# Optimization experiments

Measured on AMD Instinct MI355X. Metric: run time of the kernel, lower is better.

## Reference

```python
import jax, jax.numpy as jnp
import numpy as np

B, DIM_IN, DIM_OUT, K, SPK, T = 16, 256, 256, 5, 128, 8192
PAD = (K // 2, K // 2)  # odd kernel -> symmetric reflect pad


def setup_inputs() -> dict:
    key = jax.random.key(0)
    k1, k2, k3, k4 = jax.random.split(key, 4)
    x = jax.random.normal(k1, (B, DIM_IN, T), dtype=jnp.float32)
    c_trg = jax.random.normal(k2, (B, SPK), dtype=jnp.float32)
    # EqualLinear params (bias_init=1, lr_mul=1; forward uses raw weight, no scale)
    style_w = jax.random.normal(k3, (DIM_IN, SPK), dtype=jnp.float32)
    style_b = jnp.ones((DIM_IN,), dtype=jnp.float32)
    # base conv weight [1, dim_out, dim_in, k]
    weight = jax.random.normal(k4, (1, DIM_OUT, DIM_IN, K), dtype=jnp.float32)
    return {"x": x, "c_trg": c_trg, "style_w": style_w, "style_b": style_b, "weight": weight}


def _modulated_conv(x, c_trg, style_w, style_b, weight):
    # style: [B, dim_in]
    s = c_trg @ style_w.T + style_b
    # modulate: [B, dim_out, dim_in, K]
    w = weight * s[:, None, :, None]
    demod = jax.lax.rsqrt(jnp.sum(w * w, axis=(2, 3)) + 1e-8)  # [B, dim_out]
    w = w * demod[:, :, None, None]
    # reflect pad along time
    x_pad = jnp.pad(x, ((0, 0), (0, 0), PAD), mode="reflect")
    # per-sample conv1d (groups=batch in torch) via vmap
    def conv_one(xi, wi):
        # xi: [dim_in, T+K-1], wi: [dim_out, dim_in, K]
        out = jax.lax.conv_general_dilated(
            xi[None], wi, window_strides=(1,), padding="VALID",
            dimension_numbers=("NCH", "OIH", "NCH"))
        return out[0]  # [dim_out, T]
    out = jax.vmap(conv_one)(x_pad, w)
    return jax.nn.leaky_relu(out, negative_slope=0.2)


def reference(x, c_trg, style_w, style_b, weight):
    out = _modulated_conv(x, c_trg, style_w, style_b, weight)
    return (out, c_trg)
```

## Files before the change

kernel.cpp:

```cpp
#include <hip/hip_runtime.h>


#define B_    16
#define CIN   256
#define COUT  256
#define KW    5
#define SPK   128
#define TT    8192

#define OM    128
#define TN    256
#define BI    32
#define NCH   (CIN / BI)

#define XROWS 264
#define WSLAB (KW * OM * 32)
#define WBF_BYTES ((size_t)2 * NCH * WSLAB * 2)
#define S_OFF   WBF_BYTES
#define DM_OFF  (WBF_BYTES + (size_t)B_ * CIN * 4)
#define WS_NEED (WBF_BYTES + (size_t)B_ * CIN * 4 * 2)

typedef __attribute__((ext_vector_type(8))) short short8;
typedef __attribute__((ext_vector_type(4))) float f32x4;
typedef unsigned short ushort_t;
typedef unsigned int uint_t;

__device__ __forceinline__ ushort_t f2bf(float f) {
    uint_t u = __float_as_uint(f);
    u += 0x7FFF + ((u >> 16) & 1);
    return (ushort_t)(u >> 16);
}

__global__ __launch_bounds__(256) void prep2_kernel(
    const float* __restrict__ c_trg, const float* __restrict__ style_w,
    const float* __restrict__ style_b, const float* __restrict__ weight,
    ushort_t* __restrict__ wbf, float* __restrict__ s_glob,
    float* __restrict__ dm_glob)
{
    __shared__ float sm[8 * 1280];
    __shared__ float c_sh[SPK];
    __shared__ float s2_sh[CIN];

    const int tid = threadIdx.x;

    if (blockIdx.x < 32) {
        const int og = blockIdx.x;
        const float* wsrc = weight + (size_t)og * 8 * 1280;
        #pragma unroll
        for (int it = 0; it < 10; ++it)
            *(float4*)&sm[(it * 256 + tid) * 4] = *(const float4*)&wsrc[(it * 256 + tid) * 4];
        __syncthreads();

        for (int r = tid; r < 320; r += 256) {
            const int oi  = r / 40;
            const int rem = r - oi * 40;
            const int ch  = rem / 5;
            const int k   = rem - ch * 5;
            const int o   = og * 8 + oi;
            const int ot  = o >> 7;
            const int o_l = o & 127;
            const int swz = (o_l >> 1) & 3;
            ushort_t* dst = wbf + (((size_t)(ot * NCH + ch) * KW + k) * OM + o_l) * 32;
            #pragma unroll
            for (int g = 0; g < 4; ++g) {
                union { ushort_t us[8]; uint4 v; } pk;
                #pragma unroll
                for (int ii = 0; ii < 8; ++ii) {
                    int i_g = ch * 32 + g * 8 + ii;
                    pk.us[ii] = f2bf(sm[oi * 1280 + i_g * 5 + k]);
                }
                *(uint4*)&dst[(g ^ swz) * 8] = pk.v;
            }
        }
    } else {
        const int b = blockIdx.x - 32;
        if (tid < SPK) c_sh[tid] = c_trg[b * SPK + tid];
        __syncthreads();

        float acc = style_b[tid];
        const float* wr = style_w + (size_t)tid * SPK;
        #pragma unroll 4
        for (int j = 0; j < SPK; ++j) acc += c_sh[j] * wr[j];
        s_glob[b * CIN + tid] = acc;
        s2_sh[tid] = acc * acc;
        __syncthreads();

        const float* wo = weight + (size_t)tid * 1280;
        float a = 0.f;
        #pragma unroll 4
        for (int ig = 0; ig < 64; ++ig) {
            float q[20];
            #pragma unroll
            for (int f = 0; f < 5; ++f)
                *(float4*)&q[f * 4] = *(const float4*)&wo[ig * 20 + f * 4];
            #pragma unroll
            for (int c = 0; c < 4; ++c) {
                const float s2 = s2_sh[ig * 4 + c];
                #pragma unroll
                for (int k = 0; k < 5; ++k) {
                    const float v = q[c * 5 + k];
                    a += v * v * s2;
                }
            }
        }
        dm_glob[b * COUT + tid] = rsqrtf(a + 1e-8f);
    }
}

__global__ __launch_bounds__(512, 2) void conv_mfma_ws4_kernel(
    const float* __restrict__ x, const ushort_t* __restrict__ wbf,
    const float* __restrict__ s_glob, const float* __restrict__ dm_glob,
    float* __restrict__ out)
{
    __shared__ __align__(16) ushort_t w_sh[2][WSLAB];
    __shared__ __align__(16) ushort_t x_sh[XROWS * 32];
    __shared__ float s_lds[CIN];
    __shared__ float dm_lds[OM];

    const int b   = blockIdx.z;
    const int ot  = blockIdx.y;
    const int o0  = ot * OM;
    const int t0  = blockIdx.x * TN;
    const int tid = threadIdx.x;

    const int lane  = tid & 63;
    const int wv    = tid >> 6;
    const int wm    = wv >> 2;
    const int wn    = wv & 3;
    const int col16 = lane & 15;
    const int quad  = lane >> 4;

    const int rl = lane;
    const int i4 = wv;

    f32x4 acc[4][4];
    #pragma unroll
    for (int mt = 0; mt < 4; ++mt)
        #pragma unroll
        for (int nt = 0; nt < 4; ++nt)
            acc[mt][nt] = (f32x4){0.f, 0.f, 0.f, 0.f};

    const float* xb = x + (size_t)b * CIN * TT;
    const ushort_t* wslab = wbf + (size_t)ot * NCH * WSLAB;

    float xr0[20], xr1[20];

#define STAGE_W(CH, BUF) do {                                                  \
        const ushort_t* ws_ = wslab + (size_t)(CH) * WSLAB;                    \
        _Pragma("unroll")                                                      \
        for (int s_ = 0; s_ < 5; ++s_) {                                       \
            const int off_ = s_ * 4096 + wv * 512;           \
            __builtin_amdgcn_global_load_lds(                                  \
                (const __attribute__((address_space(1))) uint_t*)(ws_ + off_ + lane * 8), \
                (__attribute__((address_space(3))) uint_t*)(&w_sh[BUF][off_]), \
                16, 0, 0);                                                     \
        }                                                                      \
    } while (0)

#define LOAD_X(CH, XR) do {                                                    \
        const float* xp_ = xb + (size_t)((CH) * BI + i4 * 4) * TT;             \
        _Pragma("unroll")                                                      \
        for (int rd_ = 0; rd_ < 5; ++rd_) {                                    \
            int r_ = rd_ * 64 + rl;                                            \
            if (r_ < 260) {                                                    \
                int tg_ = t0 + r_ - 2;                                         \
                tg_ = (tg_ < 0) ? -tg_ : tg_;                                  \
                tg_ = (tg_ > TT - 1) ? (2 * (TT - 1) - tg_) : tg_;             \
                XR[rd_ * 4 + 0] = xp_[tg_];                                    \
                XR[rd_ * 4 + 1] = xp_[TT + tg_];                               \
                XR[rd_ * 4 + 2] = xp_[2 * TT + tg_];                           \
                XR[rd_ * 4 + 3] = xp_[3 * TT + tg_];                           \
            }                                                                  \
        }                                                                      \
    } while (0)

#define PUT_X(CH, XR) do {                                                     \
        const float s0_ = s_lds[(CH) * BI + i4 * 4 + 0];                       \
        const float s1_ = s_lds[(CH) * BI + i4 * 4 + 1];                       \
        const float s2_ = s_lds[(CH) * BI + i4 * 4 + 2];                       \
        const float s3_ = s_lds[(CH) * BI + i4 * 4 + 3];                       \
        _Pragma("unroll")                                                      \
        for (int rd_ = 0; rd_ < 5; ++rd_) {                                    \
            int r_ = rd_ * 64 + rl;                                            \
            if (r_ < 260) {                                                    \
                union { ushort_t us[4]; uint2 u2; } p_;                        \
                p_.us[0] = f2bf(XR[rd_ * 4 + 0] * s0_);                        \
                p_.us[1] = f2bf(XR[rd_ * 4 + 1] * s1_);                        \
                p_.us[2] = f2bf(XR[rd_ * 4 + 2] * s2_);                        \
                p_.us[3] = f2bf(XR[rd_ * 4 + 3] * s3_);                        \
                int grp_ = (i4 >> 1) ^ ((r_ ^ (r_ >> 2)) & 3);                 \
                *(uint2*)&x_sh[r_ * 32 + grp_ * 8 + (i4 & 1) * 4] = p_.u2;     \
            }                                                                  \
        }                                                                      \
    } while (0)

#define MFMA_CHUNK(BUF) do {                                                   \
        _Pragma("unroll")                                                      \
        for (int kt_ = 0; kt_ < KW; ++kt_) {                                   \
            short8 a_[4], bf_[4];                                              \
            _Pragma("unroll")                                                  \
            for (int mt_ = 0; mt_ < 4; ++mt_) {                                \
                const int row_  = kt_ * OM + wm * 64 + mt_ * 16 + col16;       \
                const int slot_ = quad ^ ((row_ >> 1) & 3);                    \
                a_[mt_] = *(const short8*)&w_sh[BUF][row_ * 32 + slot_ * 8];   \
            }                                                                  \
            _Pragma("unroll")                                                  \
            for (int nt_ = 0; nt_ < 4; ++nt_) {                                \
                const int r_   = wn * 64 + nt_ * 16 + col16 + kt_;             \
                const int grp_ = quad ^ ((r_ ^ (r_ >> 2)) & 3);                \
                bf_[nt_] = *(const short8*)&x_sh[r_ * 32 + grp_ * 8];          \
            }                                                                  \
            _Pragma("unroll")                                                  \
            for (int mt_ = 0; mt_ < 4; ++mt_)                                  \
                _Pragma("unroll")                                              \
                for (int nt_ = 0; nt_ < 4; ++nt_)                              \
                    acc[mt_][nt_] = __builtin_amdgcn_mfma_f32_16x16x32_bf16(   \
                        a_[mt_], bf_[nt_], acc[mt_][nt_], 0, 0, 0);            \
        }                                                                      \
    } while (0)

#define CHUNK_BODY(CH, CUR, NXT, XR_CUR, XR_NXT) do {                          \
        PUT_X(CH, XR_CUR);                                                     \
        __syncthreads();                                                       \
        if ((CH) < NCH - 1) {                                                  \
            STAGE_W((CH) + 1, NXT);                                            \
            LOAD_X((CH) + 1, XR_NXT);                                          \
        }                                                                      \
        __builtin_amdgcn_sched_barrier(0);                                     \
        MFMA_CHUNK(CUR);                                                       \
        if ((CH) < NCH - 1)                                                    \
            __syncthreads();                                                   \
    } while (0)

    if (tid < CIN) s_lds[tid] = s_glob[b * CIN + tid];
    if (tid < OM)  dm_lds[tid] = dm_glob[b * COUT + o0 + tid];
    STAGE_W(0, 0);
    LOAD_X(0, xr0);
    __syncthreads();

    CHUNK_BODY(0, 0, 1, xr0, xr1);
    CHUNK_BODY(1, 1, 0, xr1, xr0);
    CHUNK_BODY(2, 0, 1, xr0, xr1);
    CHUNK_BODY(3, 1, 0, xr1, xr0);
    CHUNK_BODY(4, 0, 1, xr0, xr1);
    CHUNK_BODY(5, 1, 0, xr1, xr0);
    CHUNK_BODY(6, 0, 1, xr0, xr1);
    CHUNK_BODY(7, 1, 0, xr1, xr0);

#undef STAGE_W
#undef LOAD_X
#undef PUT_X
#undef MFMA_CHUNK
#undef CHUNK_BODY

    #pragma unroll
    for (int mt = 0; mt < 4; ++mt) {
        #pragma unroll
        for (int nt = 0; nt < 4; ++nt) {
            const int t_o = t0 + wn * 64 + nt * 16 + col16;
            #pragma unroll
            for (int reg = 0; reg < 4; ++reg) {
                const int o_l = wm * 64 + mt * 16 + quad * 4 + reg;
                float v = acc[mt][nt][reg] * dm_lds[o_l];
                v = (v > 0.f) ? v : 0.2f * v;
                out[((size_t)(b * COUT + o0 + o_l)) * TT + t_o] = v;
            }
        }
    }
}

__global__ __launch_bounds__(256, 3) void conv_mfma_fb_kernel(
    const float* __restrict__ x, const float* __restrict__ c_trg,
    const float* __restrict__ style_w, const float* __restrict__ style_b,
    const float* __restrict__ weight, float* __restrict__ out)
{
    __shared__ ushort_t x_sh[136 * 32];
    __shared__ ushort_t w_sh[KW * 128 * 32];
    __shared__ float    c_sh[SPK];
    __shared__ float    s_sh[CIN];
    __shared__ float    dm_acc[128];
    __shared__ float    dmv[128];

    const int b   = blockIdx.z;
    const int o0  = blockIdx.y * 128;
    const int t0  = blockIdx.x * 128;
    const int tid = threadIdx.x;

    const int lane  = tid & 63;
    const int wvv   = tid >> 6;
    const int wm    = wvv >> 1;
    const int wn    = wvv & 1;
    const int col16 = lane & 15;
    const int quad  = lane >> 4;

    if (tid < SPK) c_sh[tid] = c_trg[b * SPK + tid];
    if (tid < 128) dm_acc[tid] = 0.f;
    __syncthreads();
    {
        float acc = style_b[tid];
        const float* wr = style_w + (size_t)tid * SPK;
        #pragma unroll 4
        for (int j = 0; j < SPK; ++j) acc += c_sh[j] * wr[j];
        s_sh[tid] = acc;
    }

    f32x4 acc[4][4];
    #pragma unroll
    for (int mt = 0; mt < 4; ++mt)
        #pragma unroll
        for (int nt = 0; nt < 4; ++nt)
            acc[mt][nt] = (f32x4){0.f, 0.f, 0.f, 0.f};

    const float* xb = x + (size_t)b * CIN * TT;

    for (int ch = 0; ch < NCH; ++ch) {
        const int i0 = ch * BI;
        __syncthreads();
        {
            const int i4s = tid >> 5;
            const int rls = tid & 31;
            const float* xp = xb + (size_t)(i0 + i4s * 4) * TT;
            #pragma unroll
            for (int rr = 0; rr < 136; rr += 32) {
                int r = rr + rls;
                if (r < 136) {
                    int tg = t0 + r - 2;
                    tg = (tg < 0) ? -tg : tg;
                    tg = (tg > TT - 1) ? (2 * (TT - 1) - tg) : tg;
                    float v0 = xp[tg];
                    float v1 = xp[TT + tg];
                    float v2 = xp[2 * TT + tg];
                    float v3 = xp[3 * TT + tg];
                    union { ushort_t us[4]; uint2 u2; } p;
                    p.us[0] = f2bf(v0); p.us[1] = f2bf(v1);
                    p.us[2] = f2bf(v2); p.us[3] = f2bf(v3);
                    int grp = (i4s >> 1) ^ (r & 3);
                    *(uint2*)&x_sh[r * 32 + grp * 8 + (i4s & 1) * 4] = p.u2;
                }
            }
        }
        {
            const int i4s = tid & 7;
            #pragma unroll
            for (int pass = 0; pass < 4; ++pass) {
                const int o_l = (tid >> 3) + pass * 32;
                const float* wp = weight + ((size_t)(o0 + o_l) * CIN + i0 + i4s * 4) * KW;
                float q[20];
                #pragma unroll
                for (int f = 0; f < 5; ++f)
                    *(float4*)&q[f * 4] = *(const float4*)(wp + f * 4);
                float sv0 = s_sh[i0 + i4s * 4 + 0];
                float sv1 = s_sh[i0 + i4s * 4 + 1];
                float sv2 = s_sh[i0 + i4s * 4 + 2];
                float sv3 = s_sh[i0 + i4s * 4 + 3];
                float m0[5], m1[5], m2[5], m3[5];
                float psum = 0.f;
                #pragma unroll
                for (int k = 0; k < 5; ++k) {
                    m0[k] = q[0 * 5 + k] * sv0;  psum += m0[k] * m0[k];
                    m1[k] = q[1 * 5 + k] * sv1;  psum += m1[k] * m1[k];
                    m2[k] = q[2 * 5 + k] * sv2;  psum += m2[k] * m2[k];
                    m3[k] = q[3 * 5 + k] * sv3;  psum += m3[k] * m3[k];
                }
                atomicAdd(&dm_acc[o_l], psum);
                #pragma unroll
                for (int k = 0; k < 5; ++k) {
                    union { ushort_t us[4]; uint2 u2; } p;
                    p.us[0] = f2bf(m0[k]); p.us[1] = f2bf(m1[k]);
                    p.us[2] = f2bf(m2[k]); p.us[3] = f2bf(m3[k]);
                    *(uint2*)&w_sh[(k * 128 + o_l) * 32 + i4s * 4] = p.u2;
                }
            }
        }
        __syncthreads();
        #pragma unroll
        for (int kt = 0; kt < KW; ++kt) {
            short8 a[4], bf[4];
            #pragma unroll
            for (int mt = 0; mt < 4; ++mt)
                a[mt] = *(const short8*)&w_sh[(kt * 128 + wm * 64 + mt * 16 + col16) * 32 + quad * 8];
            #pragma unroll
            for (int nt = 0; nt < 4; ++nt) {
                int r   = wn * 64 + nt * 16 + col16 + kt;
                int grp = quad ^ (r & 3);
                bf[nt] = *(const short8*)&x_sh[r * 32 + grp * 8];
            }
            #pragma unroll
            for (int mt = 0; mt < 4; ++mt)
                #pragma unroll
                for (int nt = 0; nt < 4; ++nt)
                    acc[mt][nt] = __builtin_amdgcn_mfma_f32_16x16x32_bf16(
                        a[mt], bf[nt], acc[mt][nt], 0, 0, 0);
        }
    }

    __syncthreads();
    if (tid < 128) dmv[tid] = rsqrtf(dm_acc[tid] + 1e-8f);
    __syncthreads();

    #pragma unroll
    for (int mt = 0; mt < 4; ++mt) {
        #pragma unroll
        for (int nt = 0; nt < 4; ++nt) {
            const int t_o = t0 + wn * 64 + nt * 16 + col16;
            #pragma unroll
            for (int reg = 0; reg < 4; ++reg) {
                const int o_l = wm * 64 + mt * 16 + quad * 4 + reg;
                float v = acc[mt][nt][reg] * dmv[o_l];
                v = (v > 0.f) ? v : 0.2f * v;
                out[((size_t)(b * COUT + o0 + o_l)) * TT + t_o] = v;
            }
        }
    }
}

extern "C" void kernel_launch(void* const* d_in, const int* in_sizes, int n_in,
                              void* d_out, int out_size, void* d_ws, size_t ws_size,
                              hipStream_t stream)
{
    const float* x       = (const float*)d_in[0];
    const float* c_trg   = (const float*)d_in[1];
    const float* style_w = (const float*)d_in[2];
    const float* style_b = (const float*)d_in[3];
    const float* weight  = (const float*)d_in[4];
    float* out = (float*)d_out;

    if (ws_size >= WS_NEED) {
        ushort_t* wbf   = (ushort_t*)d_ws;
        float* s_glob   = (float*)((char*)d_ws + S_OFF);
        float* dm_glob  = (float*)((char*)d_ws + DM_OFF);
        prep2_kernel<<<dim3(48), dim3(256), 0, stream>>>(
            c_trg, style_w, style_b, weight, wbf, s_glob, dm_glob);
        conv_mfma_ws4_kernel<<<dim3(TT / TN, COUT / OM, B_), dim3(512), 0, stream>>>(
            x, wbf, s_glob, dm_glob, out);
    } else {
        conv_mfma_fb_kernel<<<dim3(TT / 128, COUT / 128, B_), dim3(256), 0, stream>>>(
            x, c_trg, style_w, style_b, weight, out);
    }

    hipMemcpyAsync(out + (size_t)B_ * COUT * TT, c_trg,
                   (size_t)B_ * SPK * sizeof(float),
                   hipMemcpyDeviceToDevice, stream);
}
```

Before: 336.6 us.

## Read bf16 weights directly from global memory, drop LDS weight staging and prefetch

Removes the double-buffered LDS weight slabs and the register prefetch of x. Each wave now loads its MFMA A-fragments straight from global (L2-cached) memory, with the prep swizzle removed to match. x is loaded, scaled and stored into LDS inside the same chunk. This cuts LDS use and register pressure so launch bounds can ask for 4 blocks per CU, trading software pipelining for occupancy-based latency hiding, at the risk of exposed global-load latency in the MFMA loop.

```diff
diff --git a/kernel.cpp b/kernel.cpp
--- a/kernel.cpp
+++ b/kernel.cpp
@@ -59,7 +59,6 @@
             const int o   = og * 8 + oi;
             const int ot  = o >> 7;
             const int o_l = o & 127;
-            const int swz = (o_l >> 1) & 3;
             ushort_t* dst = wbf + (((size_t)(ot * NCH + ch) * KW + k) * OM + o_l) * 32;
             #pragma unroll
             for (int g = 0; g < 4; ++g) {
@@ -69,7 +68,7 @@
                     int i_g = ch * 32 + g * 8 + ii;
                     pk.us[ii] = f2bf(sm[oi * 1280 + i_g * 5 + k]);
                 }
-                *(uint4*)&dst[(g ^ swz) * 8] = pk.v;
+                *(uint4*)&dst[g * 8] = pk.v;
             }
         }
     } else {
@@ -107,12 +106,11 @@
     }
 }
 
-__global__ __launch_bounds__(512, 2) void conv_mfma_ws4_kernel(
+__global__ __launch_bounds__(512, 4) void conv_mfma_ws5_kernel(
     const float* __restrict__ x, const ushort_t* __restrict__ wbf,
     const float* __restrict__ s_glob, const float* __restrict__ dm_glob,
     float* __restrict__ out)
 {
-    __shared__ __align__(16) ushort_t w_sh[2][WSLAB];
     __shared__ __align__(16) ushort_t x_sh[XROWS * 32];
     __shared__ float s_lds[CIN];
     __shared__ float dm_lds[OM];
@@ -141,117 +139,63 @@
             acc[mt][nt] = (f32x4){0.f, 0.f, 0.f, 0.f};
 
     const float* xb = x + (size_t)b * CIN * TT;
-    const ushort_t* wslab = wbf + (size_t)ot * NCH * WSLAB;
-
-    float xr0[20], xr1[20];
-
-#define STAGE_W(CH, BUF) do {                                                  \
-        const ushort_t* ws_ = wslab + (size_t)(CH) * WSLAB;                    \
-        _Pragma("unroll")                                                      \
-        for (int s_ = 0; s_ < 5; ++s_) {                                       \
-            const int off_ = s_ * 4096 + wv * 512;           \
-            __builtin_amdgcn_global_load_lds(                                  \
-                (const __attribute__((address_space(1))) uint_t*)(ws_ + off_ + lane * 8), \
-                (__attribute__((address_space(3))) uint_t*)(&w_sh[BUF][off_]), \
-                16, 0, 0);                                                     \
-        }                                                                      \
-    } while (0)
-
-#define LOAD_X(CH, XR) do {                                                    \
-        const float* xp_ = xb + (size_t)((CH) * BI + i4 * 4) * TT;             \
-        _Pragma("unroll")                                                      \
-        for (int rd_ = 0; rd_ < 5; ++rd_) {                                    \
-            int r_ = rd_ * 64 + rl;                                            \
-            if (r_ < 260) {                                                    \
-                int tg_ = t0 + r_ - 2;                                         \
-                tg_ = (tg_ < 0) ? -tg_ : tg_;                                  \
-                tg_ = (tg_ > TT - 1) ? (2 * (TT - 1) - tg_) : tg_;             \
-                XR[rd_ * 4 + 0] = xp_[tg_];                                    \
-                XR[rd_ * 4 + 1] = xp_[TT + tg_];                               \
-                XR[rd_ * 4 + 2] = xp_[2 * TT + tg_];                           \
-                XR[rd_ * 4 + 3] = xp_[3 * TT + tg_];                           \
-            }                                                                  \
-        }                                                                      \
-    } while (0)
-
-#define PUT_X(CH, XR) do {                                                     \
-        const float s0_ = s_lds[(CH) * BI + i4 * 4 + 0];                       \
-        const float s1_ = s_lds[(CH) * BI + i4 * 4 + 1];                       \
-        const float s2_ = s_lds[(CH) * BI + i4 * 4 + 2];                       \
-        const float s3_ = s_lds[(CH) * BI + i4 * 4 + 3];                       \
-        _Pragma("unroll")                                                      \
-        for (int rd_ = 0; rd_ < 5; ++rd_) {                                    \
-            int r_ = rd_ * 64 + rl;                                            \
-            if (r_ < 260) {                                                    \
-                union { ushort_t us[4]; uint2 u2; } p_;                        \
-                p_.us[0] = f2bf(XR[rd_ * 4 + 0] * s0_);                        \
-                p_.us[1] = f2bf(XR[rd_ * 4 + 1] * s1_);                        \
-                p_.us[2] = f2bf(XR[rd_ * 4 + 2] * s2_);                        \
-                p_.us[3] = f2bf(XR[rd_ * 4 + 3] * s3_);                        \
-                int grp_ = (i4 >> 1) ^ ((r_ ^ (r_ >> 2)) & 3);                 \
-                *(uint2*)&x_sh[r_ * 32 + grp_ * 8 + (i4 & 1) * 4] = p_.u2;     \
-            }                                                                  \
-        }                                                                      \
-    } while (0)
-
-#define MFMA_CHUNK(BUF) do {                                                   \
-        _Pragma("unroll")                                                      \
-        for (int kt_ = 0; kt_ < KW; ++kt_) {                                   \
-            short8 a_[4], bf_[4];                                              \
-            _Pragma("unroll")                                                  \
-            for (int mt_ = 0; mt_ < 4; ++mt_) {                                \
-                const int row_  = kt_ * OM + wm * 64 + mt_ * 16 + col16;       \
-                const int slot_ = quad ^ ((row_ >> 1) & 3);                    \
-                a_[mt_] = *(const short8*)&w_sh[BUF][row_ * 32 + slot_ * 8];   \
-            }                                                                  \
-            _Pragma("unroll")                                                  \
-            for (int nt_ = 0; nt_ < 4; ++nt_) {                                \
-                const int r_   = wn * 64 + nt_ * 16 + col16 + kt_;             \
-                const int grp_ = quad ^ ((r_ ^ (r_ >> 2)) & 3);                \
-                bf_[nt_] = *(const short8*)&x_sh[r_ * 32 + grp_ * 8];          \
-            }                                                                  \
-            _Pragma("unroll")                                                  \
-            for (int mt_ = 0; mt_ < 4; ++mt_)                                  \
-                _Pragma("unroll")                                              \
-                for (int nt_ = 0; nt_ < 4; ++nt_)                              \
-                    acc[mt_][nt_] = __builtin_amdgcn_mfma_f32_16x16x32_bf16(   \
-                        a_[mt_], bf_[nt_], acc[mt_][nt_], 0, 0, 0);            \
-        }                                                                      \
-    } while (0)
-
-#define CHUNK_BODY(CH, CUR, NXT, XR_CUR, XR_NXT) do {                          \
-        PUT_X(CH, XR_CUR);                                                     \
-        __syncthreads();                                                       \
-        if ((CH) < NCH - 1) {                                                  \
-            STAGE_W((CH) + 1, NXT);                                            \
-            LOAD_X((CH) + 1, XR_NXT);                                          \
-        }                                                                      \
-        __builtin_amdgcn_sched_barrier(0);                                     \
-        MFMA_CHUNK(CUR);                                                       \
-        if ((CH) < NCH - 1)                                                    \
-            __syncthreads();                                                   \
-    } while (0)
+    const ushort_t* wbase = wbf + (size_t)ot * NCH * WSLAB
+                          + ((size_t)(wm * 64 + col16)) * 32 + quad * 8;
 
     if (tid < CIN) s_lds[tid] = s_glob[b * CIN + tid];
     if (tid < OM)  dm_lds[tid] = dm_glob[b * COUT + o0 + tid];
-    STAGE_W(0, 0);
-    LOAD_X(0, xr0);
     __syncthreads();
 
-    CHUNK_BODY(0, 0, 1, xr0, xr1);
-    CHUNK_BODY(1, 1, 0, xr1, xr0);
-    CHUNK_BODY(2, 0, 1, xr0, xr1);
-    CHUNK_BODY(3, 1, 0, xr1, xr0);
-    CHUNK_BODY(4, 0, 1, xr0, xr1);
-    CHUNK_BODY(5, 1, 0, xr1, xr0);
-    CHUNK_BODY(6, 0, 1, xr0, xr1);
-    CHUNK_BODY(7, 1, 0, xr1, xr0);
-
-#undef STAGE_W
-#undef LOAD_X
-#undef PUT_X
-#undef MFMA_CHUNK
-#undef CHUNK_BODY
+    for (int ch = 0; ch < NCH; ++ch) {
+        {
+            const float s0 = s_lds[ch * BI + i4 * 4 + 0];
+            const float s1 = s_lds[ch * BI + i4 * 4 + 1];
+            const float s2 = s_lds[ch * BI + i4 * 4 + 2];
+            const float s3 = s_lds[ch * BI + i4 * 4 + 3];
+            const float* xp = xb + (size_t)(ch * BI + i4 * 4) * TT;
+            #pragma unroll
+            for (int rd = 0; rd < 5; ++rd) {
+                int r = rd * 64 + rl;
+                if (r < 260) {
+                    int tg = t0 + r - 2;
+                    tg = (tg < 0) ? -tg : tg;
+                    tg = (tg > TT - 1) ? (2 * (TT - 1) - tg) : tg;
+                    union { ushort_t us[4]; uint2 u2; } p;
+                    p.us[0] = f2bf(xp[tg] * s0);
+                    p.us[1] = f2bf(xp[TT + tg] * s1);
+                    p.us[2] = f2bf(xp[2 * TT + tg] * s2);
+                    p.us[3] = f2bf(xp[3 * TT + tg] * s3);
+                    int grp = (i4 >> 1) ^ ((r ^ (r >> 2)) & 3);
+                    *(uint2*)&x_sh[r * 32 + grp * 8 + (i4 & 1) * 4] = p.u2;
+                }
+            }
+        }
+        __syncthreads();
+
+        const ushort_t* wch = wbase + (size_t)ch * WSLAB;
+        #pragma unroll
+        for (int kt = 0; kt < KW; ++kt) {
+            short8 a[4], bf[4];
+            #pragma unroll
+            for (int mt = 0; mt < 4; ++mt)
+                a[mt] = *(const short8*)&wch[((size_t)kt * OM + mt * 16) * 32];
+            #pragma unroll
+            for (int nt = 0; nt < 4; ++nt) {
+                const int r   = wn * 64 + nt * 16 + col16 + kt;
+                const int grp = quad ^ ((r ^ (r >> 2)) & 3);
+                bf[nt] = *(const short8*)&x_sh[r * 32 + grp * 8];
+            }
+            #pragma unroll
+            for (int mt = 0; mt < 4; ++mt)
+                #pragma unroll
+                for (int nt = 0; nt < 4; ++nt)
+                    acc[mt][nt] = __builtin_amdgcn_mfma_f32_16x16x32_bf16(
+                        a[mt], bf[nt], acc[mt][nt], 0, 0, 0);
+        }
+
+        if (ch < NCH - 1)
+            __syncthreads();
+    }
 
     #pragma unroll
     for (int mt = 0; mt < 4; ++mt) {
@@ -431,7 +375,7 @@
         float* dm_glob  = (float*)((char*)d_ws + DM_OFF);
         prep2_kernel<<<dim3(48), dim3(256), 0, stream>>>(
             c_trg, style_w, style_b, weight, wbf, s_glob, dm_glob);
-        conv_mfma_ws4_kernel<<<dim3(TT / TN, COUT / OM, B_), dim3(512), 0, stream>>>(
+        conv_mfma_ws5_kernel<<<dim3(TT / TN, COUT / OM, B_), dim3(512), 0, stream>>>(
             x, wbf, s_glob, dm_glob, out);
     } else {
         conv_mfma_fb_kernel<<<dim3(TT / 128, COUT / 128, B_), dim3(256), 0, stream>>>(
```

After: 418.0 us. +24.2%, slower.
